# Performance work log

Measured on AMD Instinct MI355X. Metric: run time of the kernel, lower is better.

Reference implementation:

```python
import jax, jax.numpy as jnp
import numpy as np

EPS = 1e-6  # config.norm_eps


def setup_inputs() -> dict:
    key = jax.random.key(0)
    k1, k2 = jax.random.split(key)
    n, B, T, D = 8, 4, 2048, 2048
    V = jax.random.normal(k1, (n, B, T, D), dtype=jnp.float32)
    key_norm_weight = jnp.ones((D,), dtype=jnp.float32)  # RMSNorm gain for this step_idx
    pseudo_query = jax.random.normal(k2, (D,), dtype=jnp.float32)
    return {"V": V, "key_norm_weight": key_norm_weight, "pseudo_query": pseudo_query}


def reference(V, key_norm_weight, pseudo_query):
    # V: (n, B, T, D) stacked block representations
    # RMSNorm over last dim (key_norms[step_idx](V))
    rms = jax.lax.rsqrt(jnp.mean(V * V, axis=-1, keepdims=True) + EPS)
    K = V * rms * key_norm_weight  # (n, B, T, D)
    # scalar logits per depth entry: einsum('d, n b t d -> n b t')
    logits = jnp.einsum('nbtd,d->nbt', K, pseudo_query)
    # softmax over depth axis n
    weights = jax.nn.softmax(logits, axis=0)  # (n, B, T)
    # weighted combination: einsum('n b t, n b t d -> b t d')
    return jnp.einsum('nbt,nbtd->btd', weights, V)
```

## Files before the change

### kernel.cpp

```cpp
#include <hip/hip_runtime.h>

#define NDEPTH 8
#define DDIM 2048
#define THREADS 512
#define EPS 1e-6f

typedef float f32x4 __attribute__((ext_vector_type(4)));

__global__ __launch_bounds__(THREADS)
void block_attn_residual_kernel(const float* __restrict__ V,
                                const float* __restrict__ wn,
                                const float* __restrict__ pq,
                                float* __restrict__ out,
                                int BT) {
    const int bt  = blockIdx.x;
    const int tid = threadIdx.x;
    const int f   = tid;

    const f32x4* w4 = reinterpret_cast<const f32x4*>(wn);
    const f32x4* q4 = reinterpret_cast<const f32x4*>(pq);
    const f32x4 wv = w4[f];
    const f32x4 qv = q4[f];
    const f32x4 wq = wv * qv;

    const f32x4* V4 = reinterpret_cast<const f32x4*>(V) + (size_t)bt * (DDIM / 4);
    const size_t nStride = (size_t)BT * (DDIM / 4);

    f32x4 v[NDEPTH];
    float ss[NDEPTH];
    float dt[NDEPTH];

#pragma unroll
    for (int n = 0; n < NDEPTH; ++n) {
        f32x4 x = __builtin_nontemporal_load(&V4[(size_t)n * nStride + f]);
        v[n] = x;
        ss[n] = x[0]*x[0] + x[1]*x[1] + x[2]*x[2] + x[3]*x[3];
        dt[n] = x[0]*wq[0] + x[1]*wq[1] + x[2]*wq[2] + x[3]*wq[3];
    }

#pragma unroll
    for (int n = 0; n < NDEPTH; ++n) {
#pragma unroll
        for (int off = 32; off > 0; off >>= 1) {
            ss[n] += __shfl_xor(ss[n], off, 64);
            dt[n] += __shfl_xor(dt[n], off, 64);
        }
    }

    __shared__ float red_ss[8][NDEPTH];
    __shared__ float red_dt[8][NDEPTH];
    const int wave = tid >> 6;
    const int lane = tid & 63;
    if (lane == 0) {
#pragma unroll
        for (int n = 0; n < NDEPTH; ++n) {
            red_ss[wave][n] = ss[n];
            red_dt[wave][n] = dt[n];
        }
    }
    __syncthreads();

    float logit[NDEPTH];
    float m = -INFINITY;
#pragma unroll
    for (int n = 0; n < NDEPTH; ++n) {
        float S = 0.0f, Dq = 0.0f;
#pragma unroll
        for (int w = 0; w < 8; ++w) {
            S  += red_ss[w][n];
            Dq += red_dt[w][n];
        }
        float rms = rsqrtf(S * (1.0f / DDIM) + EPS);
        logit[n] = rms * Dq;
        m = fmaxf(m, logit[n]);
    }
    float wgt[NDEPTH];
    float denom = 0.0f;
#pragma unroll
    for (int n = 0; n < NDEPTH; ++n) {
        wgt[n] = __expf(logit[n] - m);
        denom += wgt[n];
    }
    const float inv = 1.0f / denom;

    f32x4 o = {0.0f, 0.0f, 0.0f, 0.0f};
#pragma unroll
    for (int n = 0; n < NDEPTH; ++n) {
        const float wn_ = wgt[n] * inv;
        o[0] += wn_ * v[n][0];
        o[1] += wn_ * v[n][1];
        o[2] += wn_ * v[n][2];
        o[3] += wn_ * v[n][3];
    }

    f32x4* out4 = reinterpret_cast<f32x4*>(out) + (size_t)bt * (DDIM / 4);
    __builtin_nontemporal_store(o, &out4[f]);
}

extern "C" void kernel_launch(void* const* d_in, const int* in_sizes, int n_in,
                              void* d_out, int out_size, void* d_ws, size_t ws_size,
                              hipStream_t stream) {
    const float* V  = (const float*)d_in[0];
    const float* wn = (const float*)d_in[1];
    const float* pq = (const float*)d_in[2];
    float* out = (float*)d_out;

    const int BT = in_sizes[0] / (NDEPTH * DDIM);
    block_attn_residual_kernel<<<dim3(BT), dim3(THREADS), 0, stream>>>(V, wn, pq, out, BT);
}
```

Baseline: 105.8 us.

## Use transpose-style butterfly reduction and single-wave softmax to cut shuffles

Replaces 16 independent full-wave butterfly reductions (96 shuffles) with a recursive-halving reduction that packs the 16 partial sums so each shuffle stage halves the live values, needing far fewer cross-lane ops. The cross-wave combine and softmax are then done by wave 0 alone with vector LDS reads and 8-lane shuffles, and the normalized weights are broadcast through shared memory. This adds a second barrier and more select logic. The kernel is likely memory-bound, so the shuffle savings may not show up in the timing.

```diff
diff --git a/kernel.cpp b/kernel.cpp
--- a/kernel.cpp
+++ b/kernel.cpp
@@ -13,85 +13,102 @@
                                 const float* __restrict__ pq,
                                 float* __restrict__ out,
                                 int BT) {
-    const int bt  = blockIdx.x;
-    const int tid = threadIdx.x;
-    const int f   = tid;
+    const int bt   = blockIdx.x;
+    const int tid  = threadIdx.x;
+    const int f    = tid;
+    const int wave = tid >> 6;
+    const int lane = tid & 63;
+
+    __shared__ __align__(16) float red[16][NDEPTH];
+    __shared__ __align__(16) float wgt8[NDEPTH];
 
     const f32x4* w4 = reinterpret_cast<const f32x4*>(wn);
     const f32x4* q4 = reinterpret_cast<const f32x4*>(pq);
-    const f32x4 wv = w4[f];
-    const f32x4 qv = q4[f];
-    const f32x4 wq = wv * qv;
+    const f32x4 wq = w4[f] * q4[f];
 
     const f32x4* V4 = reinterpret_cast<const f32x4*>(V) + (size_t)bt * (DDIM / 4);
     const size_t nStride = (size_t)BT * (DDIM / 4);
 
     f32x4 v[NDEPTH];
-    float ss[NDEPTH];
-    float dt[NDEPTH];
+    float val[16];
 
 #pragma unroll
     for (int n = 0; n < NDEPTH; ++n) {
         f32x4 x = __builtin_nontemporal_load(&V4[(size_t)n * nStride + f]);
         v[n] = x;
-        ss[n] = x[0]*x[0] + x[1]*x[1] + x[2]*x[2] + x[3]*x[3];
-        dt[n] = x[0]*wq[0] + x[1]*wq[1] + x[2]*wq[2] + x[3]*wq[3];
+        val[n]     = x[0]*x[0]  + x[1]*x[1]  + x[2]*x[2]  + x[3]*x[3];
+        val[n + 8] = x[0]*wq[0] + x[1]*wq[1] + x[2]*wq[2] + x[3]*wq[3];
     }
 
 #pragma unroll
-    for (int n = 0; n < NDEPTH; ++n) {
+    for (int i = 0; i < 8; ++i) {
+        float a = val[i], b = val[i + 8];
+        float x = (lane & 32) ? a : b;
+        float y = __shfl_xor(x, 32, 64);
+        val[i] = ((lane & 32) ? b : a) + y;
+    }
 #pragma unroll
-        for (int off = 32; off > 0; off >>= 1) {
-            ss[n] += __shfl_xor(ss[n], off, 64);
-            dt[n] += __shfl_xor(dt[n], off, 64);
+    for (int i = 0; i < 4; ++i) {
+        float a = val[i], b = val[i + 4];
+        float x = (lane & 16) ? a : b;
+        float y = __shfl_xor(x, 16, 64);
+        val[i] = ((lane & 16) ? b : a) + y;
+    }
+#pragma unroll
+    for (int i = 0; i < 2; ++i) {
+        float a = val[i], b = val[i + 2];
+        float x = (lane & 8) ? a : b;
+        float y = __shfl_xor(x, 8, 64);
+        val[i] = ((lane & 8) ? b : a) + y;
+    }
+    {
+        float a = val[0], b = val[1];
+        float x = (lane & 4) ? a : b;
+        float y = __shfl_xor(x, 4, 64);
+        val[0] = ((lane & 4) ? b : a) + y;
+    }
+    float t = val[0];
+    t += __shfl_xor(t, 2, 64);
+    t += __shfl_xor(t, 1, 64);
+
+    if ((lane & 3) == 0) red[(lane >> 2) & 15][wave] = t;
+    __syncthreads();
+
+    if (wave == 0) {
+        float tot = 0.0f;
+        if (lane < 16) {
+            const f32x4* r4 = reinterpret_cast<const f32x4*>(&red[lane][0]);
+            f32x4 p = r4[0] + r4[1];
+            tot = p[0] + p[1] + p[2] + p[3];
         }
-    }
-
-    __shared__ float red_ss[8][NDEPTH];
-    __shared__ float red_dt[8][NDEPTH];
-    const int wave = tid >> 6;
-    const int lane = tid & 63;
-    if (lane == 0) {
-#pragma unroll
-        for (int n = 0; n < NDEPTH; ++n) {
-            red_ss[wave][n] = ss[n];
-            red_dt[wave][n] = dt[n];
-        }
+        float dq = __shfl(tot, (lane & 7) + 8, 64);
+        float rms = rsqrtf(tot * (1.0f / DDIM) + EPS);
+        float logit = rms * dq;
+        float m = logit;
+        m = fmaxf(m, __shfl_xor(m, 1, 8));
+        m = fmaxf(m, __shfl_xor(m, 2, 8));
+        m = fmaxf(m, __shfl_xor(m, 4, 8));
+        float e = __expf(logit - m);
+        float s = e;
+        s += __shfl_xor(s, 1, 8);
+        s += __shfl_xor(s, 2, 8);
+        s += __shfl_xor(s, 4, 8);
+        if (lane < 8) wgt8[lane] = e / s;
     }
     __syncthreads();
 
-    float logit[NDEPTH];
-    float m = -INFINITY;
-#pragma unroll
-    for (int n = 0; n < NDEPTH; ++n) {
-        float S = 0.0f, Dq = 0.0f;
-#pragma unroll
-        for (int w = 0; w < 8; ++w) {
-            S  += red_ss[w][n];
-            Dq += red_dt[w][n];
-        }
-        float rms = rsqrtf(S * (1.0f / DDIM) + EPS);
-        logit[n] = rms * Dq;
-        m = fmaxf(m, logit[n]);
-    }
-    float wgt[NDEPTH];
-    float denom = 0.0f;
-#pragma unroll
-    for (int n = 0; n < NDEPTH; ++n) {
-        wgt[n] = __expf(logit[n] - m);
-        denom += wgt[n];
-    }
-    const float inv = 1.0f / denom;
+    const f32x4* wg4 = reinterpret_cast<const f32x4*>(wgt8);
+    const f32x4 wA = wg4[0];
+    const f32x4 wB = wg4[1];
 
-    f32x4 o = {0.0f, 0.0f, 0.0f, 0.0f};
-#pragma unroll
-    for (int n = 0; n < NDEPTH; ++n) {
-        const float wn_ = wgt[n] * inv;
-        o[0] += wn_ * v[n][0];
-        o[1] += wn_ * v[n][1];
-        o[2] += wn_ * v[n][2];
-        o[3] += wn_ * v[n][3];
-    }
+    f32x4 o = wA[0] * v[0];
+    o += wA[1] * v[1];
+    o += wA[2] * v[2];
+    o += wA[3] * v[3];
+    o += wB[0] * v[4];
+    o += wB[1] * v[5];
+    o += wB[2] * v[6];
+    o += wB[3] * v[7];
 
     f32x4* out4 = reinterpret_cast<f32x4*>(out) + (size_t)bt * (DDIM / 4);
     __builtin_nontemporal_store(o, &out4[f]);
```

Result: faster. 101.5 us (-4.1%).
